# Kernel optimization log

Hardware: AMD Instinct MI355X
Metric: run time of the kernel (lower is better)

## Reference

```python
import jax, jax.numpy as jnp
import numpy as np

LN_EPS = 1e-5


def _conv2d(x, w, b, pad):
    # x: [B,C,H,W], w: [O,I,k,k] (torch OIHW layout)
    out = jax.lax.conv_general_dilated(
        x, w, (1, 1), [(pad, pad), (pad, pad)],
        dimension_numbers=('NCHW', 'OIHW', 'NCHW'))
    return out + b[None, :, None, None]


def _deform_conv2d(x, offset, w, b, k, pad):
    # torchvision.ops.deform_conv2d, offset_groups=1, stride=1, dilation=1.
    # offset layout: [B, 2*k*k, H, W] with (dy, dx) interleaved per kernel tap.
    B, C, H, W = x.shape
    off = offset.reshape(B, k * k, 2, H, W)
    dy, dx = off[:, :, 0], off[:, :, 1]                      # [B,kk,H,W]
    ky, kx = jnp.meshgrid(jnp.arange(k, dtype=x.dtype),
                          jnp.arange(k, dtype=x.dtype), indexing='ij')
    py = (jnp.arange(H, dtype=x.dtype)[None, None, :, None]
          - pad + ky.reshape(-1)[None, :, None, None] + dy)   # sample rows
    px = (jnp.arange(W, dtype=x.dtype)[None, None, None, :]
          - pad + kx.reshape(-1)[None, :, None, None] + dx)   # sample cols
    y0 = jnp.floor(py)
    x0 = jnp.floor(px)
    fy = py - y0
    fx = px - x0
    xf = x.reshape(B, C, H * W)
    gather = jax.vmap(lambda xb, ib: xb[:, ib])               # [C,HW],[K]->[C,K]

    def corner(yc, xc, wt):
        valid = (yc >= 0) & (yc < H) & (xc >= 0) & (xc < W)
        idx = (jnp.clip(yc, 0, H - 1) * W
               + jnp.clip(xc, 0, W - 1)).astype(jnp.int32).reshape(B, -1)
        g = gather(xf, idx).reshape(B, C, k * k, H, W)
        return g * (wt * valid.astype(x.dtype))[:, None]

    # bilinear sample with zero padding outside the image
    acc = (corner(y0, x0, (1 - fy) * (1 - fx))
           + corner(y0, x0 + 1, (1 - fy) * fx)
           + corner(y0 + 1, x0, fy * (1 - fx))
           + corner(y0 + 1, x0 + 1, fy * fx))                 # [B,C,kk,H,W]
    out = jnp.einsum('bckhw,ock->bohw', acc, w.reshape(w.shape[0], C, k * k))
    return out + b[None, :, None, None]


def _deform_branch(xs, off_w, off_b, conv_w, conv_b, k, pad):
    # DeformableConv2d.forward: offset conv, deform_conv2d with conv's own
    # weight/bias, then the plain conv applied AGAIN on the result.
    offset = _conv2d(xs, off_w, off_b, pad)
    d = _deform_conv2d(xs, offset, conv_w, conv_b, k, pad)
    return _conv2d(d, conv_w, conv_b, pad)


def reference(x, H, W, fc1_w, fc1_b, off3_w, off3_b, conv3_w, conv3_b,
              off5_w, off5_b, conv5_w, conv5_b, ln_g, ln_b, fc2_w, fc2_b):
    B, N, _ = x.shape
    h = x @ fc1_w.T + fc1_b                                  # [B,N,hid]
    C = h.shape[-1]
    C2 = C // 2
    x1 = jnp.transpose(h[..., :C2], (0, 2, 1)).reshape(B, C2, H, W)
    x2 = jnp.transpose(h[..., C2:], (0, 2, 1)).reshape(B, C2, H, W)
    x1 = _deform_branch(x1, off3_w, off3_b, conv3_w, conv3_b, 3, 1)
    x2 = _deform_branch(x2, off5_w, off5_b, conv5_w, conv5_b, 5, 2)
    y = jnp.concatenate([x1, x2], axis=1)                    # [B,C,H,W]
    y = jnp.transpose(y.reshape(B, C, N), (0, 2, 1))         # [B,N,C]
    mu = jnp.mean(y, axis=-1, keepdims=True)
    var = jnp.mean(jnp.square(y - mu), axis=-1, keepdims=True)
    y = (y - mu) * jax.lax.rsqrt(var + LN_EPS) * ln_g + ln_b
    y = jax.nn.gelu(y, approximate=False)                    # nn.GELU default
    return y @ fc2_w.T + fc2_b


def setup_inputs() -> dict:
    key = jax.random.key(0)
    ks = jax.random.split(key, 16)
    B, H, W, Cin, Chid = 4, 32, 32, 256, 1024
    C2 = Chid // 2
    N = H * W
    r = lambda k, s, sc: jax.random.normal(k, s, dtype=jnp.float32) * sc
    return {
        'x': r(ks[0], (B, N, Cin), 1.0),
        'H': H, 'W': W,
        'fc1_w': r(ks[1], (Chid, Cin), 0.02),
        'fc1_b': r(ks[2], (Chid,), 0.02),
        'off3_w': r(ks[3], (2 * 9, C2, 3, 3), 0.01),
        'off3_b': r(ks[4], (2 * 9,), 0.01),
        'conv3_w': r(ks[5], (C2, C2, 3, 3), 0.02),
        'conv3_b': r(ks[6], (C2,), 0.02),
        'off5_w': r(ks[7], (2 * 25, C2, 5, 5), 0.01),
        'off5_b': r(ks[8], (2 * 25,), 0.01),
        'conv5_w': r(ks[9], (C2, C2, 5, 5), 0.02),
        'conv5_b': r(ks[10], (C2,), 0.02),
        'ln_g': jnp.ones((Chid,), jnp.float32),
        'ln_b': jnp.zeros((Chid,), jnp.float32),
        'fc2_w': r(ks[11], (Cin, Chid), 0.02),
        'fc2_b': r(ks[12], (Cin,), 0.02),
    }
```

## Files before the change

kernel.cpp:

```cpp
#include <hip/hip_runtime.h>

#define B_    4
#define H_    32
#define W_    32
#define N_    1024
#define CIN_  256
#define CHID_ 1024
#define C2_   512

typedef __attribute__((ext_vector_type(8))) short short8b;
typedef __attribute__((ext_vector_type(4))) float f32x4;

__device__ __forceinline__ unsigned int f2bf2(float lo, float hi) {
    unsigned int ul = __float_as_uint(lo);
    unsigned int uh = __float_as_uint(hi);
    ul += 0x7fffu + ((ul >> 16) & 1u);
    uh += 0x7fffu + ((uh >> 16) & 1u);
    return (ul >> 16) | (uh & 0xffff0000u);
}
__device__ __forceinline__ unsigned short f2bf(float f) {
    unsigned int u = __float_as_uint(f);
    u += 0x7fffu + ((u >> 16) & 1u);
    return (unsigned short)(u >> 16);
}
__device__ __forceinline__ float bflo(unsigned int u) { return __uint_as_float(u << 16); }
__device__ __forceinline__ float bfhi(unsigned int u) { return __uint_as_float(u & 0xffff0000u); }

#define ROWP 40
#define MFMA_(a, b, c) __builtin_amdgcn_mfma_f32_16x16x32_bf16(a, b, c, 0, 0, 0)

template<int AMODE, int KS, int CH, int OUTMODE, int GX>
__global__ __launch_bounds__(512, 2)
void cgemm(const void* __restrict__ Asrc, int lda,
           const unsigned short* __restrict__ Bp, int nk32,
           int tcnt, int KK,
           const float* __restrict__ bias, void* __restrict__ Cout,
           int ldo, int O, int nO16,
           const short4* __restrict__ cidx, const float4* __restrict__ cwt)
{
    __shared__ unsigned short As[2][2][64 * ROWP];

    const int tid = threadIdx.x;
    int m0, o0, tbeg, zslab;
    if constexpr (GX > 0) {
        const int bid = blockIdx.x;
        o0 = (bid & (GX - 1)) * 128;
        m0 = (bid / GX) * 64;
        tbeg = 0; zslab = 0;
    } else {
        o0 = 0;
        m0 = blockIdx.y * 64;
        zslab = blockIdx.z;
        tbeg = zslab * tcnt;
    }

    const int srow = tid >> 3;
    const int sk8  = (tid & 7) << 3;
    const int am = m0 + srow;
    const int an = am & (N_ - 1), ab = am >> 10;
    const int ay = an >> 5, ax = an & 31;

    const int lane = tid & 63, wid = tid >> 6;
    const int wr = (wid >> 2) * 32, wc = (wid & 3) * 32;
    const int l15 = lane & 15, lk = (lane >> 4) * 8;

    const int o16a = min((o0 + wc) >> 4, nO16 - 1);
    const int o16b = min((o0 + wc + 16) >> 4, nO16 - 1);
    const unsigned short* bbA = Bp + (size_t)o16a * nk32 * 512 + lane * 8;
    const unsigned short* bbB = Bp + (size_t)o16b * nk32 * 512 + lane * 8;

    const float* fp = nullptr;
    const unsigned short* sp = nullptr;
    bool svalid = false;
    const unsigned short *g0p = nullptr, *g1p = nullptr,
                         *g2p = nullptr, *g3p = nullptr;
    float4 scw = {0.f, 0.f, 0.f, 0.f};

    auto setShift = [&](int t) {
        const int PAD = KS / 2;
        const int ty = t / KS, tx = t - ty * KS;
        const int yy = ay + ty - PAD, xx = ax + tx - PAD;
        svalid = (yy >= 0 && yy < H_ && xx >= 0 && xx < W_);
        if (svalid)
            sp = (const unsigned short*)Asrc
               + (size_t)((ab << 10) | (yy << 5) | xx) * lda + sk8;
    };
    auto setGather = [&](short4 ci, float4 cw) {
        const unsigned short* base = (const unsigned short*)Asrc;
        g0p = base + (size_t)(int)ci.x * lda + sk8;
        g1p = base + (size_t)(int)ci.y * lda + sk8;
        g2p = base + (size_t)(int)ci.z * lda + sk8;
        g3p = base + (size_t)(int)ci.w * lda + sk8;
        scw = cw;
    };
    auto stage = [&](int s) -> uint4 {
        if constexpr (AMODE == 0) {
            const float* p = fp + (s << 6);
            const float4 v0 = *(const float4*)p;
            const float4 v1 = *(const float4*)(p + 4);
            return make_uint4(f2bf2(v0.x, v0.y), f2bf2(v0.z, v0.w),
                              f2bf2(v1.x, v1.y), f2bf2(v1.z, v1.w));
        } else if constexpr (AMODE == 1) {
            if (!svalid) return make_uint4(0u, 0u, 0u, 0u);
            return *(const uint4*)(sp + (s << 6));
        } else {
            const uint4 g0 = *(const uint4*)(g0p + (s << 6));
            const uint4 g1 = *(const uint4*)(g1p + (s << 6));
            const uint4 g2 = *(const uint4*)(g2p + (s << 6));
            const uint4 g3 = *(const uint4*)(g3p + (s << 6));
            const unsigned int* pa = (const unsigned int*)&g0;
            const unsigned int* pb = (const unsigned int*)&g1;
            const unsigned int* pc = (const unsigned int*)&g2;
            const unsigned int* pd = (const unsigned int*)&g3;
            uint4 out;
            unsigned int* po = (unsigned int*)&out;
#pragma unroll
            for (int j = 0; j < 4; ++j) {
                const float rl = scw.x * bflo(pa[j]) + scw.y * bflo(pb[j])
                               + scw.z * bflo(pc[j]) + scw.w * bflo(pd[j]);
                const float rh = scw.x * bfhi(pa[j]) + scw.y * bfhi(pb[j])
                               + scw.z * bfhi(pc[j]) + scw.w * bfhi(pd[j]);
                po[j] = f2bf2(rl, rh);
            }
            return out;
        }
    };

    if constexpr (AMODE == 0) fp = (const float*)Asrc + (size_t)am * lda + sk8;
    else if constexpr (AMODE == 1) setShift(tbeg);
    else setGather(cidx[(size_t)am * KK + tbeg], cwt[(size_t)am * KK + tbeg]);

    f32x4 acc[2][2];
#pragma unroll
    for (int i = 0; i < 2; ++i)
#pragma unroll
        for (int j = 0; j < 2; ++j)
            acc[i][j] = (f32x4){0.f, 0.f, 0.f, 0.f};

    {
        const uint4 v = stage(0);
        *(uint4*)&As[0][sk8 >> 5][srow * ROWP + (sk8 & 31)] = v;
    }
    const int q00 = tbeg * (2 * CH);
    short8b cA0 = *(const short8b*)(bbA + (size_t)(q00    ) * 512);
    short8b cA1 = *(const short8b*)(bbA + (size_t)(q00 + 1) * 512);
    short8b cB0 = *(const short8b*)(bbB + (size_t)(q00    ) * 512);
    short8b cB1 = *(const short8b*)(bbB + (size_t)(q00 + 1) * 512);
    __syncthreads();

    int cur = 0;

    auto step = [&](int s, int qn, bool doNext, bool newTap, int tnext,
                    short4 cin, float4 cwn) {
        short8b nA0, nA1, nB0, nB1;
        if (doNext) {
            nA0 = *(const short8b*)(bbA + (size_t)(qn    ) * 512);
            nA1 = *(const short8b*)(bbA + (size_t)(qn + 1) * 512);
            nB0 = *(const short8b*)(bbB + (size_t)(qn    ) * 512);
            nB1 = *(const short8b*)(bbB + (size_t)(qn + 1) * 512);
        }
        uint4 nv;
        if (doNext) {
            if (newTap) {
                if constexpr (AMODE == 1) setShift(tnext);
                else if constexpr (AMODE == 2) setGather(cin, cwn);
                nv = stage(0);
            } else {
                nv = stage(s + 1);
            }
        }
        const unsigned short* a0 = As[cur][0];
        const unsigned short* a1 = As[cur][1];
        const short8b af00 = *(const short8b*)(a0 + (wr      + l15) * ROWP + lk);
        const short8b af01 = *(const short8b*)(a0 + (wr + 16 + l15) * ROWP + lk);
        const short8b af10 = *(const short8b*)(a1 + (wr      + l15) * ROWP + lk);
        const short8b af11 = *(const short8b*)(a1 + (wr + 16 + l15) * ROWP + lk);

        acc[0][0] = MFMA_(af00, cA0, acc[0][0]);
        acc[0][1] = MFMA_(af00, cB0, acc[0][1]);
        acc[1][0] = MFMA_(af01, cA0, acc[1][0]);
        acc[1][1] = MFMA_(af01, cB0, acc[1][1]);
        acc[0][0] = MFMA_(af10, cA1, acc[0][0]);
        acc[0][1] = MFMA_(af10, cB1, acc[0][1]);
        acc[1][0] = MFMA_(af11, cA1, acc[1][0]);
        acc[1][1] = MFMA_(af11, cB1, acc[1][1]);

        if (doNext)
            *(uint4*)&As[cur ^ 1][sk8 >> 5][srow * ROWP + (sk8 & 31)] = nv;
        __syncthreads();
        cur ^= 1;
        cA0 = nA0; cA1 = nA1; cB0 = nB0; cB1 = nB1;
    };

    for (int ti = 0; ti + 1 < tcnt; ++ti) {
        short4 cin = {0, 0, 0, 0}; float4 cwn = {0.f, 0.f, 0.f, 0.f};
        if constexpr (AMODE == 2) {
            cin = cidx[(size_t)am * KK + tbeg + ti + 1];
            cwn = cwt [(size_t)am * KK + tbeg + ti + 1];
        }
        const int qt = (tbeg + ti) * (2 * CH);
        const int qn0 = (tbeg + ti + 1) * (2 * CH);
#pragma unroll
        for (int s = 0; s < CH; ++s) {
            const bool nt = (s == CH - 1);
            step(s, nt ? qn0 : qt + (s + 1) * 2, true, nt, tbeg + ti + 1, cin, cwn);
        }
    }
    {
        const int qt = (tbeg + tcnt - 1) * (2 * CH);
        const short4 cz = {0, 0, 0, 0}; const float4 cwz = {0.f, 0.f, 0.f, 0.f};
#pragma unroll
        for (int s = 0; s < CH; ++s)
            step(s, qt + (s + 1) * 2, s < CH - 1, false, 0, cz, cwz);
    }

    const int row0 = m0 + wr + (lane >> 4) * 4;
    const int col0 = o0 + wc + l15;
#pragma unroll
    for (int j = 0; j < 2; ++j) {
        const int cc = col0 + j * 16;
        if (cc < O) {
#pragma unroll
            for (int i = 0; i < 2; ++i)
#pragma unroll
                for (int r = 0; r < 4; ++r) {
                    const int row = row0 + i * 16 + r;
                    if constexpr (OUTMODE == 0)
                        ((float*)Cout)[(size_t)row * ldo + cc] = acc[i][j][r] + bias[cc];
                    else if constexpr (OUTMODE == 1)
                        ((unsigned short*)Cout)[(size_t)row * ldo + cc] =
                            f2bf(acc[i][j][r] + bias[cc]);
                    else
                        ((float*)Cout)[(size_t)zslab * (B_ * N_) * 64
                                       + (size_t)row * 64 + cc] = acc[i][j][r];
                }
        }
    }
}

__global__ void pack_w(const float* __restrict__ w, unsigned short* __restrict__ dst,
                       int Ovalid, int Opad, int obase, int Kc, int KK, int t0, int Ktot)
{
    const int gid = blockIdx.x * blockDim.x + threadIdx.x;
    if (gid >= Opad * Ktot) return;
    const int k  = gid % Ktot;
    const int od = gid / Ktot;
    float v = 0.f;
    if (od < Ovalid) {
        const size_t o = obase + od;
        if (KK == 1) {
            v = w[o * Kc + k];
        } else {
            const int t = t0 + (k >> 9);
            const int c = k & 511;
            v = w[(o * Kc + c) * KK + t];
        }
    }
    const int o16 = od >> 4, l = od & 15, k32 = k >> 5;
    const size_t di = ((size_t)(o16 * (Ktot >> 5) + k32) * 64
                       + (l + ((k >> 3) & 3) * 16)) * 8 + (k & 7);
    dst[di] = f2bf(v);
}

template<int KS, int Z>
__global__ void coeff_kernel(const float* __restrict__ offp,
                             const float* __restrict__ ob,
                             short4* __restrict__ cidx, float4* __restrict__ cwt)
{
    const int KK = KS * KS, PAD = KS / 2;
    const int gid = blockIdx.x * blockDim.x + threadIdx.x;
    if (gid >= B_ * N_ * KK) return;
    const int t = gid % KK;
    const int n = (gid / KK) & (N_ - 1);
    const int b = gid / (KK * N_);
    const int mtok = b * N_ + n;

    const int SL = B_ * N_ * 64;
    float dy = ob[2 * t], dx = ob[2 * t + 1];
#pragma unroll
    for (int z = 0; z < Z; ++z) {
        dy += offp[(size_t)z * SL + (size_t)mtok * 64 + 2 * t];
        dx += offp[(size_t)z * SL + (size_t)mtok * 64 + 2 * t + 1];
    }

    const int y = n >> 5, x = n & 31;
    const float py = (float)(y - PAD + t / KS) + dy;
    const float px = (float)(x - PAD + t % KS) + dx;
    const float y0f = floorf(py), x0f = floorf(px);
    const float fy = py - y0f, fx = px - x0f;
    const int y0 = (int)y0f, x0 = (int)x0f;

    int idx[4]; float wt[4];
    const int   yy[4] = {y0, y0, y0 + 1, y0 + 1};
    const int   xx[4] = {x0, x0 + 1, x0, x0 + 1};
    const float ww[4] = {(1.f - fy) * (1.f - fx), (1.f - fy) * fx,
                         fy * (1.f - fx),         fy * fx};
#pragma unroll
    for (int r = 0; r < 4; ++r) {
        const bool v = (yy[r] >= 0 && yy[r] < H_ && xx[r] >= 0 && xx[r] < W_);
        const int yc = min(max(yy[r], 0), H_ - 1);
        const int xc = min(max(xx[r], 0), W_ - 1);
        idx[r] = b * N_ + yc * W_ + xc;
        wt[r] = v ? ww[r] : 0.f;
    }
    cidx[(size_t)mtok * KK + t] =
        make_short4((short)idx[0], (short)idx[1], (short)idx[2], (short)idx[3]);
    cwt[(size_t)mtok * KK + t] = make_float4(wt[0], wt[1], wt[2], wt[3]);
}

__global__ __launch_bounds__(256)
void ln_gelu(float* __restrict__ ytok, const float* __restrict__ g,
             const float* __restrict__ bt)
{
    const int t = blockIdx.x;
    const int tid = threadIdx.x;
    float* row = ytok + (size_t)t * CHID_;

    float4 v = *(const float4*)&row[tid << 2];
    __shared__ float red[4];

    float s = v.x + v.y + v.z + v.w;
#pragma unroll
    for (int o = 32; o > 0; o >>= 1) s += __shfl_down(s, o, 64);
    if ((tid & 63) == 0) red[tid >> 6] = s;
    __syncthreads();
    const float mean = (red[0] + red[1] + red[2] + red[3]) * (1.f / CHID_);

    const float d0 = v.x - mean, d1 = v.y - mean, d2 = v.z - mean, d3 = v.w - mean;
    float q = d0 * d0 + d1 * d1 + d2 * d2 + d3 * d3;
#pragma unroll
    for (int o = 32; o > 0; o >>= 1) q += __shfl_down(q, o, 64);
    __syncthreads();
    if ((tid & 63) == 0) red[tid >> 6] = q;
    __syncthreads();
    const float var = (red[0] + red[1] + red[2] + red[3]) * (1.f / CHID_);
    const float rstd = rsqrtf(var + 1e-5f);

    const float4 gv = *(const float4*)&g[tid << 2];
    const float4 bv = *(const float4*)&bt[tid << 2];
    float o0 = d0 * rstd * gv.x + bv.x;
    float o1 = d1 * rstd * gv.y + bv.y;
    float o2 = d2 * rstd * gv.z + bv.z;
    float o3 = d3 * rstd * gv.w + bv.w;
    o0 = 0.5f * o0 * (1.f + erff(o0 * 0.70710678118654752f));
    o1 = 0.5f * o1 * (1.f + erff(o1 * 0.70710678118654752f));
    o2 = 0.5f * o2 * (1.f + erff(o2 * 0.70710678118654752f));
    o3 = 0.5f * o3 * (1.f + erff(o3 * 0.70710678118654752f));
    *(float4*)&row[tid << 2] = make_float4(o0, o1, o2, o3);
}

extern "C" void kernel_launch(void* const* d_in, const int* in_sizes, int n_in,
                              void* d_out, int out_size, void* d_ws, size_t ws_size,
                              hipStream_t stream) {
    const float* x       = (const float*)d_in[0];
    const float* fc1_w   = (const float*)d_in[3];
    const float* fc1_b   = (const float*)d_in[4];
    const float* off3_w  = (const float*)d_in[5];
    const float* off3_b  = (const float*)d_in[6];
    const float* conv3_w = (const float*)d_in[7];
    const float* conv3_b = (const float*)d_in[8];
    const float* off5_w  = (const float*)d_in[9];
    const float* off5_b  = (const float*)d_in[10];
    const float* conv5_w = (const float*)d_in[11];
    const float* conv5_b = (const float*)d_in[12];
    const float* ln_g    = (const float*)d_in[13];
    const float* ln_b    = (const float*)d_in[14];
    const float* fc2_w   = (const float*)d_in[15];
    const float* fc2_b   = (const float*)d_in[16];
    float* out = (float*)d_out;

    char* ws = (char*)d_ws;
    float*          ytok   = (float*)(ws);
    float*          offp   = (float*)(ws);
    short4*         cidx3  = (short4*)(ws + 5242880);
    float4*         cwt3   = (float4*)(ws + 5537792);
    short4*         cidx5  = (short4*)(ws + 16777216);
    float4*         cwt5   = (float4*)(ws + 17596416);
    unsigned short* hb     = (unsigned short*)(ws + 19234816);
    unsigned short* fc1wb  = (unsigned short*)(ws + 27623424);
    unsigned short* off3wb = (unsigned short*)(ws + 28147712);
    unsigned short* off5wb = (unsigned short*)(ws + 28737536);
    unsigned short* daccb  = (unsigned short*)(ws + 27623424);
    unsigned short* fc2wb  = (unsigned short*)(ws + 31817728);
    unsigned short* conv3wb= (unsigned short*)(ws + 32342016);
    unsigned short* conv5wb= (unsigned short*)(ws + 37060608);

    const dim3 TB(256);
    const dim3 TG(512);

    pack_w<<<(1024*256  + 255)/256, TB, 0, stream>>>(fc1_w,  fc1wb,  1024, 1024, 0, 256, 1, 0, 256);
    pack_w<<<(256*1024  + 255)/256, TB, 0, stream>>>(fc2_w,  fc2wb,  256,  256,  0, 1024, 1, 0, 1024);
    pack_w<<<(64*4608   + 255)/256, TB, 0, stream>>>(off3_w, off3wb, 18,   64,   0, 512, 9, 0, 4608);
    pack_w<<<(64*12800  + 255)/256, TB, 0, stream>>>(off5_w, off5wb, 50,   64,   0, 512, 25, 0, 12800);
    pack_w<<<(512*4608  + 255)/256, TB, 0, stream>>>(conv3_w, conv3wb, 512, 512, 0, 512, 9, 0, 4608);
    pack_w<<<(512*12800 + 255)/256, TB, 0, stream>>>(conv5_w, conv5wb, 512, 512, 0, 512, 25, 0, 12800);

    cgemm<0,1,4,1,8><<<8*64, TG, 0, stream>>>(
        x, CIN_, fc1wb, 8, 1, 1, fc1_b, hb, CHID_, CHID_, 64, nullptr, nullptr);

    cgemm<1,3,8,2,0><<<dim3(1,64,3), TG, 0, stream>>>(
        hb, CHID_, off3wb, 144, 3, 1, nullptr, offp, 64, 18, 4, nullptr, nullptr);
    coeff_kernel<3,3><<<(B_*N_*9 + 255)/256, TB, 0, stream>>>(offp, off3_b, cidx3, cwt3);
    cgemm<1,5,8,2,0><<<dim3(1,64,5), TG, 0, stream>>>(
        hb + C2_, CHID_, off5wb, 400, 5, 1, nullptr, offp, 64, 50, 4, nullptr, nullptr);
    coeff_kernel<5,5><<<(B_*N_*25 + 255)/256, TB, 0, stream>>>(offp, off5_b, cidx5, cwt5);

    cgemm<2,3,8,1,4><<<4*64, TG, 0, stream>>>(
        hb, CHID_, conv3wb, 144, 9, 9, conv3_b, daccb, C2_, C2_, 32, cidx3, cwt3);
    cgemm<1,3,8,0,4><<<4*64, TG, 0, stream>>>(
        daccb, C2_, conv3wb, 144, 9, 1, conv3_b, ytok, CHID_, C2_, 32, nullptr, nullptr);

    cgemm<2,5,8,1,4><<<4*64, TG, 0, stream>>>(
        hb + C2_, CHID_, conv5wb, 400, 25, 25, conv5_b, daccb, C2_, C2_, 32, cidx5, cwt5);
    cgemm<1,5,8,0,4><<<4*64, TG, 0, stream>>>(
        daccb, C2_, conv5wb, 400, 25, 1, conv5_b, ytok + C2_, CHID_, C2_, 32, nullptr, nullptr);

    ln_gelu<<<B_*N_, TB, 0, stream>>>(ytok, ln_g, ln_b);
    cgemm<0,1,16,0,2><<<2*64, TG, 0, stream>>>(
        ytok, CHID_, fc2wb, 32, 1, 1, fc2_b, out, CIN_, CIN_, 16, nullptr, nullptr);
}
```

Measured before the change: 696.1 us.

## Deepen GEMM A-operand prefetch to two stages and add faster conv weight packer

```diff
diff --git a/kernel.cpp b/kernel.cpp
--- a/kernel.cpp
+++ b/kernel.cpp
@@ -28,6 +28,12 @@
 
 #define ROWP 40
 #define MFMA_(a, b, c) __builtin_amdgcn_mfma_f32_16x16x32_bf16(a, b, c, 0, 0, 0)
+
+template<int X> struct Log2 { static constexpr int v = 1 + Log2<X/2>::v; };
+template<> struct Log2<1> { static constexpr int v = 0; };
+
+struct ASet { uint4 r0, r1, r2, r3; float4 cw; };
+struct BSet { short8b b0, b1, b2, b3; };
 
 template<int AMODE, int KS, int CH, int OUTMODE, int GX>
 __global__ __launch_bounds__(512, 2)
@@ -38,6 +44,7 @@
            int ldo, int O, int nO16,
            const short4* __restrict__ cidx, const float4* __restrict__ cwt)
 {
+    constexpr int CHS = Log2<CH>::v;
     __shared__ unsigned short As[2][2][64 * ROWP];
 
     const int tid = threadIdx.x;
@@ -69,66 +76,95 @@
     const unsigned short* bbA = Bp + (size_t)o16a * nk32 * 512 + lane * 8;
     const unsigned short* bbB = Bp + (size_t)o16b * nk32 * 512 + lane * 8;
 
+    const int T = tcnt << CHS;
+    const int qbase = (tbeg << CHS) * 2;
+
     const float* fp = nullptr;
     const unsigned short* sp = nullptr;
     bool svalid = false;
     const unsigned short *g0p = nullptr, *g1p = nullptr,
                          *g2p = nullptr, *g3p = nullptr;
-    float4 scw = {0.f, 0.f, 0.f, 0.f};
-
-    auto setShift = [&](int t) {
-        const int PAD = KS / 2;
-        const int ty = t / KS, tx = t - ty * KS;
-        const int yy = ay + ty - PAD, xx = ax + tx - PAD;
-        svalid = (yy >= 0 && yy < H_ && xx >= 0 && xx < W_);
-        if (svalid)
-            sp = (const unsigned short*)Asrc
-               + (size_t)((ab << 10) | (yy << 5) | xx) * lda + sk8;
-    };
-    auto setGather = [&](short4 ci, float4 cw) {
-        const unsigned short* base = (const unsigned short*)Asrc;
-        g0p = base + (size_t)(int)ci.x * lda + sk8;
-        g1p = base + (size_t)(int)ci.y * lda + sk8;
-        g2p = base + (size_t)(int)ci.z * lda + sk8;
-        g3p = base + (size_t)(int)ci.w * lda + sk8;
-        scw = cw;
-    };
-    auto stage = [&](int s) -> uint4 {
+    float4 curCw = {0.f, 0.f, 0.f, 0.f};
+    short4 ciPref = {0, 0, 0, 0};
+    float4 cwPref = {0.f, 0.f, 0.f, 0.f};
+
+    if constexpr (AMODE == 0) {
+        fp = (const float*)Asrc + (size_t)am * lda + sk8;
+    } else if constexpr (AMODE == 2) {
+        ciPref = cidx[(size_t)am * KK + tbeg];
+        cwPref = cwt [(size_t)am * KK + tbeg];
+    }
+
+    auto advanceTap = [&](int tp) {
+        if constexpr (AMODE == 1) {
+            const int PAD = KS / 2;
+            const int ty = tp / KS, tx = tp - ty * KS;
+            const int yy = ay + ty - PAD, xx = ax + tx - PAD;
+            svalid = (yy >= 0 && yy < H_ && xx >= 0 && xx < W_);
+            if (svalid)
+                sp = (const unsigned short*)Asrc
+                   + (size_t)((ab << 10) | (yy << 5) | xx) * lda + sk8;
+        } else if constexpr (AMODE == 2) {
+            const unsigned short* base = (const unsigned short*)Asrc;
+            g0p = base + (size_t)(int)ciPref.x * lda + sk8;
+            g1p = base + (size_t)(int)ciPref.y * lda + sk8;
+            g2p = base + (size_t)(int)ciPref.z * lda + sk8;
+            g3p = base + (size_t)(int)ciPref.w * lda + sk8;
+            curCw = cwPref;
+            ciPref = cidx[(size_t)am * KK + tp + 1];
+            cwPref = cwt [(size_t)am * KK + tp + 1];
+        }
+    };
+
+    auto loadRaw = [&](ASet& S, int u) {
         if constexpr (AMODE == 0) {
-            const float* p = fp + (s << 6);
-            const float4 v0 = *(const float4*)p;
-            const float4 v1 = *(const float4*)(p + 4);
-            return make_uint4(f2bf2(v0.x, v0.y), f2bf2(v0.z, v0.w),
-                              f2bf2(v1.x, v1.y), f2bf2(v1.z, v1.w));
+            S.r0 = *(const uint4*)(fp + (u << 6));
+            S.r1 = *(const uint4*)(fp + (u << 6) + 4);
         } else if constexpr (AMODE == 1) {
-            if (!svalid) return make_uint4(0u, 0u, 0u, 0u);
-            return *(const uint4*)(sp + (s << 6));
+            S.r0 = svalid ? *(const uint4*)(sp + (u << 6))
+                          : make_uint4(0u, 0u, 0u, 0u);
         } else {
-            const uint4 g0 = *(const uint4*)(g0p + (s << 6));
-            const uint4 g1 = *(const uint4*)(g1p + (s << 6));
-            const uint4 g2 = *(const uint4*)(g2p + (s << 6));
-            const uint4 g3 = *(const uint4*)(g3p + (s << 6));
-            const unsigned int* pa = (const unsigned int*)&g0;
-            const unsigned int* pb = (const unsigned int*)&g1;
-            const unsigned int* pc = (const unsigned int*)&g2;
-            const unsigned int* pd = (const unsigned int*)&g3;
-            uint4 out;
-            unsigned int* po = (unsigned int*)&out;
-#pragma unroll
-            for (int j = 0; j < 4; ++j) {
-                const float rl = scw.x * bflo(pa[j]) + scw.y * bflo(pb[j])
-                               + scw.z * bflo(pc[j]) + scw.w * bflo(pd[j]);
-                const float rh = scw.x * bfhi(pa[j]) + scw.y * bfhi(pb[j])
-                               + scw.z * bfhi(pc[j]) + scw.w * bfhi(pd[j]);
-                po[j] = f2bf2(rl, rh);
-            }
-            return out;
-        }
-    };
-
-    if constexpr (AMODE == 0) fp = (const float*)Asrc + (size_t)am * lda + sk8;
-    else if constexpr (AMODE == 1) setShift(tbeg);
-    else setGather(cidx[(size_t)am * KK + tbeg], cwt[(size_t)am * KK + tbeg]);
+            S.r0 = *(const uint4*)(g0p + (u << 6));
+            S.r1 = *(const uint4*)(g1p + (u << 6));
+            S.r2 = *(const uint4*)(g2p + (u << 6));
+            S.r3 = *(const uint4*)(g3p + (u << 6));
+            S.cw = curCw;
+        }
+    };
+
+    auto bl1 = [](unsigned a, unsigned b, unsigned c, unsigned d, float4 cw) {
+        const float lo = cw.x * bflo(a) + cw.y * bflo(b)
+                       + cw.z * bflo(c) + cw.w * bflo(d);
+        const float hi = cw.x * bfhi(a) + cw.y * bfhi(b)
+                       + cw.z * bfhi(c) + cw.w * bfhi(d);
+        return f2bf2(lo, hi);
+    };
+
+    auto blendWrite = [&](ASet& S, int buf) {
+        uint4 o;
+        if constexpr (AMODE == 0) {
+            o = make_uint4(f2bf2(__uint_as_float(S.r0.x), __uint_as_float(S.r0.y)),
+                           f2bf2(__uint_as_float(S.r0.z), __uint_as_float(S.r0.w)),
+                           f2bf2(__uint_as_float(S.r1.x), __uint_as_float(S.r1.y)),
+                           f2bf2(__uint_as_float(S.r1.z), __uint_as_float(S.r1.w)));
+        } else if constexpr (AMODE == 1) {
+            o = S.r0;
+        } else {
+            o = make_uint4(bl1(S.r0.x, S.r1.x, S.r2.x, S.r3.x, S.cw),
+                           bl1(S.r0.y, S.r1.y, S.r2.y, S.r3.y, S.cw),
+                           bl1(S.r0.z, S.r1.z, S.r2.z, S.r3.z, S.cw),
+                           bl1(S.r0.w, S.r1.w, S.r2.w, S.r3.w, S.cw));
+        }
+        *(uint4*)&As[buf][sk8 >> 5][srow * ROWP + (sk8 & 31)] = o;
+    };
+
+    auto loadB = [&](BSet& Bv, int g) {
+        const int q = qbase + 2 * g;
+        Bv.b0 = *(const short8b*)(bbA + (size_t)q * 512);
+        Bv.b1 = *(const short8b*)(bbA + (size_t)(q + 1) * 512);
+        Bv.b2 = *(const short8b*)(bbB + (size_t)q * 512);
+        Bv.b3 = *(const short8b*)(bbB + (size_t)(q + 1) * 512);
+    };
 
     f32x4 acc[2][2];
 #pragma unroll
@@ -137,38 +173,29 @@
         for (int j = 0; j < 2; ++j)
             acc[i][j] = (f32x4){0.f, 0.f, 0.f, 0.f};
 
+    ASet S0, S1; BSet B0, B1;
+
+    advanceTap(tbeg);
     {
-        const uint4 v = stage(0);
-        *(uint4*)&As[0][sk8 >> 5][srow * ROWP + (sk8 & 31)] = v;
-    }
-    const int q00 = tbeg * (2 * CH);
-    short8b cA0 = *(const short8b*)(bbA + (size_t)(q00    ) * 512);
-    short8b cA1 = *(const short8b*)(bbA + (size_t)(q00 + 1) * 512);
-    short8b cB0 = *(const short8b*)(bbB + (size_t)(q00    ) * 512);
-    short8b cB1 = *(const short8b*)(bbB + (size_t)(q00 + 1) * 512);
+        ASet P;
+        loadRaw(P, 0);
+        blendWrite(P, 0);
+    }
+    loadRaw(S0, 1);
+    loadB(B0, 0);
     __syncthreads();
 
     int cur = 0;
 
-    auto step = [&](int s, int qn, bool doNext, bool newTap, int tnext,
-                    short4 cin, float4 cwn) {
-        short8b nA0, nA1, nB0, nB1;
-        if (doNext) {
-            nA0 = *(const short8b*)(bbA + (size_t)(qn    ) * 512);
-            nA1 = *(const short8b*)(bbA + (size_t)(qn + 1) * 512);
-            nB0 = *(const short8b*)(bbB + (size_t)(qn    ) * 512);
-            nB1 = *(const short8b*)(bbB + (size_t)(qn + 1) * 512);
-        }
-        uint4 nv;
-        if (doNext) {
-            if (newTap) {
-                if constexpr (AMODE == 1) setShift(tnext);
-                else if constexpr (AMODE == 2) setGather(cin, cwn);
-                nv = stage(0);
-            } else {
-                nv = stage(s + 1);
-            }
-        }
+    auto iter = [&](int g, ASet& N, ASet& F, BSet& bc, BSet& bn) {
+        if (g + 1 < T) loadB(bn, g + 1);
+        if (g + 2 < T) {
+            const int gn = g + 2;
+            if ((gn & (CH - 1)) == 0) advanceTap(tbeg + (gn >> CHS));
+            loadRaw(F, gn & (CH - 1));
+        }
+        if (g + 1 < T) blendWrite(N, cur ^ 1);
+
         const unsigned short* a0 = As[cur][0];
         const unsigned short* a1 = As[cur][1];
         const short8b af00 = *(const short8b*)(a0 + (wr      + l15) * ROWP + lk);
@@ -176,42 +203,22 @@
         const short8b af10 = *(const short8b*)(a1 + (wr      + l15) * ROWP + lk);
         const short8b af11 = *(const short8b*)(a1 + (wr + 16 + l15) * ROWP + lk);
 
-        acc[0][0] = MFMA_(af00, cA0, acc[0][0]);
-        acc[0][1] = MFMA_(af00, cB0, acc[0][1]);
-        acc[1][0] = MFMA_(af01, cA0, acc[1][0]);
-        acc[1][1] = MFMA_(af01, cB0, acc[1][1]);
-        acc[0][0] = MFMA_(af10, cA1, acc[0][0]);
-        acc[0][1] = MFMA_(af10, cB1, acc[0][1]);
-        acc[1][0] = MFMA_(af11, cA1, acc[1][0]);
-        acc[1][1] = MFMA_(af11, cB1, acc[1][1]);
-
-        if (doNext)
-            *(uint4*)&As[cur ^ 1][sk8 >> 5][srow * ROWP + (sk8 & 31)] = nv;
+        acc[0][0] = MFMA_(af00, bc.b0, acc[0][0]);
+        acc[0][1] = MFMA_(af00, bc.b2, acc[0][1]);
+        acc[1][0] = MFMA_(af01, bc.b0, acc[1][0]);
+        acc[1][1] = MFMA_(af01, bc.b2, acc[1][1]);
+        acc[0][0] = MFMA_(af10, bc.b1, acc[0][0]);
+        acc[0][1] = MFMA_(af10, bc.b3, acc[0][1]);
+        acc[1][0] = MFMA_(af11, bc.b1, acc[1][0]);
+        acc[1][1] = MFMA_(af11, bc.b3, acc[1][1]);
+
         __syncthreads();
         cur ^= 1;
-        cA0 = nA0; cA1 = nA1; cB0 = nB0; cB1 = nB1;
-    };
-
-    for (int ti = 0; ti + 1 < tcnt; ++ti) {
-        short4 cin = {0, 0, 0, 0}; float4 cwn = {0.f, 0.f, 0.f, 0.f};
-        if constexpr (AMODE == 2) {
-            cin = cidx[(size_t)am * KK + tbeg + ti + 1];
-            cwn = cwt [(size_t)am * KK + tbeg + ti + 1];
-        }
-        const int qt = (tbeg + ti) * (2 * CH);
-        const int qn0 = (tbeg + ti + 1) * (2 * CH);
-#pragma unroll
-        for (int s = 0; s < CH; ++s) {
-            const bool nt = (s == CH - 1);
-            step(s, nt ? qn0 : qt + (s + 1) * 2, true, nt, tbeg + ti + 1, cin, cwn);
-        }
-    }
-    {
-        const int qt = (tbeg + tcnt - 1) * (2 * CH);
-        const short4 cz = {0, 0, 0, 0}; const float4 cwz = {0.f, 0.f, 0.f, 0.f};
-#pragma unroll
-        for (int s = 0; s < CH; ++s)
-            step(s, qt + (s + 1) * 2, s < CH - 1, false, 0, cz, cwz);
+    };
+
+    for (int g = 0; g < T; g += 2) {
+        iter(g,     S0, S1, B0, B1);
+        iter(g + 1, S1, S0, B1, B0);
     }
 
     const int row0 = m0 + wr + (lane >> 4) * 4;
@@ -260,6 +267,27 @@
     const size_t di = ((size_t)(o16 * (Ktot >> 5) + k32) * 64
                        + (l + ((k >> 3) & 3) * 16)) * 8 + (k & 7);
     dst[di] = f2bf(v);
+}
+
+__global__ void pack_conv(const float* __restrict__ w, unsigned short* __restrict__ dst,
+                          int O, int KK)
+{
+    const int gid = blockIdx.x * blockDim.x + threadIdx.x;
+    if (gid >= O * 256) return;
+    const int c2 = gid & 255;
+    const int o  = gid >> 8;
+    const int c  = c2 << 1;
+    const float* src = w + ((size_t)o * 512 + c) * KK;
+    const int nk32 = KK << 4;
+    const int o16 = o >> 4, l = o & 15;
+    for (int t = 0; t < KK; ++t) {
+        const float v0 = src[t];
+        const float v1 = src[KK + t];
+        const int k = t * 512 + c;
+        const size_t di = ((size_t)(o16 * nk32 + (k >> 5)) * 64
+                           + (l + ((k >> 3) & 3) * 16)) * 8 + (k & 7);
+        *(unsigned int*)&dst[di] = f2bf2(v0, v1);
+    }
 }
 
 template<int KS, int Z>
@@ -388,12 +416,12 @@
     const dim3 TB(256);
     const dim3 TG(512);
 
-    pack_w<<<(1024*256  + 255)/256, TB, 0, stream>>>(fc1_w,  fc1wb,  1024, 1024, 0, 256, 1, 0, 256);
-    pack_w<<<(256*1024  + 255)/256, TB, 0, stream>>>(fc2_w,  fc2wb,  256,  256,  0, 1024, 1, 0, 1024);
-    pack_w<<<(64*4608   + 255)/256, TB, 0, stream>>>(off3_w, off3wb, 18,   64,   0, 512, 9, 0, 4608);
-    pack_w<<<(64*12800  + 255)/256, TB, 0, stream>>>(off5_w, off5wb, 50,   64,   0, 512, 25, 0, 12800);
-    pack_w<<<(512*4608  + 255)/256, TB, 0, stream>>>(conv3_w, conv3wb, 512, 512, 0, 512, 9, 0, 4608);
-    pack_w<<<(512*12800 + 255)/256, TB, 0, stream>>>(conv5_w, conv5wb, 512, 512, 0, 512, 25, 0, 12800);
+    pack_w<<<(1024*256 + 255)/256, TB, 0, stream>>>(fc1_w, fc1wb, 1024, 1024, 0, 256, 1, 0, 256);
+    pack_w<<<(256*1024 + 255)/256, TB, 0, stream>>>(fc2_w, fc2wb, 256, 256, 0, 1024, 1, 0, 1024);
+    pack_w<<<(64*4608  + 255)/256, TB, 0, stream>>>(off3_w, off3wb, 18, 64, 0, 512, 9, 0, 4608);
+    pack_w<<<(64*12800 + 255)/256, TB, 0, stream>>>(off5_w, off5wb, 50, 64, 0, 512, 25, 0, 12800);
+    pack_conv<<<(512*256 + 255)/256, TB, 0, stream>>>(conv3_w, conv3wb, 512, 9);
+    pack_conv<<<(512*256 + 255)/256, TB, 0, stream>>>(conv5_w, conv5wb, 512, 25);
 
     cgemm<0,1,4,1,8><<<8*64, TG, 0, stream>>>(
         x, CIN_, fc1wb, 8, 1, 1, fc1_b, hb, CHID_, CHID_, 64, nullptr, nullptr);
```

After: 699.5 us. Within noise of the previous version (+0.5%).
